# Kernel tuning notes

Hardware: AMD Instinct MI355X
Metric: run time of the kernel (lower is better)

Reference implementation:

```python
import jax, jax.numpy as jnp
import numpy as np
from jax import lax

# Shared Conv2d [1,1] + BN + ReLU is represented as a per-point affine (BN folded
# into conv weight/bias at eval) followed by ReLU, matching inference-mode math.

B, N1, N2, K = 8, 8192, 2048, 8
C1, C2 = 64, 128
MLP0, MLP1, MLP2 = 128, 128, 128  # mlp=[128,128], mlp2=[128]


def setup_inputs() -> dict:
    key = jax.random.key(0)
    ks = jax.random.split(key, 10)
    sc = lambda fan_in: 1.0 / np.sqrt(fan_in)
    return {
        "xyz1": jax.random.normal(ks[0], (B, N1, 3), jnp.float32),
        "xyz2": jax.random.normal(ks[1], (B, N2, 3), jnp.float32),
        "feat1": jax.random.normal(ks[2], (B, N1, C1), jnp.float32),
        "feat2": jax.random.normal(ks[3], (B, N2, C2), jnp.float32),
        "W0": jax.random.normal(ks[4], (C2 + 3, MLP0), jnp.float32) * sc(C2 + 3),
        "b0": jnp.zeros((MLP0,), jnp.float32),
        "W1": jax.random.normal(ks[5], (MLP0, MLP1), jnp.float32) * sc(MLP0),
        "b1": jnp.zeros((MLP1,), jnp.float32),
        "W2": jax.random.normal(ks[6], (MLP1 + C1, MLP2), jnp.float32) * sc(MLP1 + C1),
        "b2": jnp.zeros((MLP2,), jnp.float32),
    }


def _knn_idx(xyz1, xyz2, k):
    # squared distances (B, N1, N2); top-k nearest in xyz2 for each xyz1 point
    d2 = jnp.sum((xyz1[:, :, None, :] - xyz2[:, None, :, :]) ** 2, axis=-1)
    _, idx = lax.top_k(-d2, k)  # (B, N1, K)
    return idx


def _gather(src, idx):
    # src: (B, N2, C), idx: (B, N1, K) -> (B, N1, K, C)
    return jax.vmap(lambda s, i: s[i])(src, idx)


def reference(xyz1, xyz2, feat1, feat2, W0, b0, W1, b1, W2, b2):
    idx = _knn_idx(xyz1, xyz2, K)
    xyz2_g = _gather(xyz2, idx)            # (B, N1, K, 3)
    feat2_g = _gather(feat2, idx)          # (B, N1, K, C2)
    xyz_diff = xyz2_g - xyz1[:, :, None, :]
    net = jnp.concatenate([feat2_g, xyz_diff], axis=-1)  # (B, N1, K, C2+3)
    net = jax.nn.relu(net @ W0 + b0)
    net = jax.nn.relu(net @ W1 + b1)       # (B, N1, K, MLP1)
    pooled = jnp.max(net, axis=2)          # max pooling over neighbors
    cat = jnp.concatenate([pooled, feat1], axis=-1)      # (B, N1, MLP1+C1)
    out = jax.nn.relu(cat @ W2 + b2)       # (B, N1, MLP2)
    return out
```

## Files before the change

kernel.cpp:

```cpp
#include <hip/hip_runtime.h>
#include <hip/hip_bf16.h>

constexpr int B_  = 8;
constexpr int N1_ = 8192;
constexpr int N2_ = 2048;
constexpr int K_  = 8;

typedef short bf16x8 __attribute__((ext_vector_type(8)));
typedef float f32x4  __attribute__((ext_vector_type(4)));
typedef float f32x2  __attribute__((ext_vector_type(2)));

__device__ __forceinline__ short f2b(float x) {
    __hip_bfloat16 h = __float2bfloat16(x);
    return *reinterpret_cast<short*>(&h);
}

#define CASF(a, b) { const float _lo = fminf(a, b); \
                     const float _hi = fmaxf(a, b); \
                     (a) = _lo; (b) = _hi; }

__global__ __launch_bounds__(256) void prep_all(
    const float* __restrict__ feat2, short* __restrict__ feat2b,
    const float* __restrict__ W0, const float* __restrict__ W1,
    const float* __restrict__ W2, const float* __restrict__ xyz2,
    short* __restrict__ W0T, short* __restrict__ W1T, short* __restrict__ W2T,
    float* __restrict__ xp) {
    if (blockIdx.x < 2048) {
        const int i = blockIdx.x * 256 + threadIdx.x;
        const float4 v = ((const float4*)feat2)[i];
        uint2 o;
        o.x = (unsigned short)f2b(v.x) | ((unsigned)(unsigned short)f2b(v.y) << 16);
        o.y = (unsigned short)f2b(v.z) | ((unsigned)(unsigned short)f2b(v.w) << 16);
        ((uint2*)feat2b)[i] = o;
        return;
    }
    int i = (blockIdx.x - 2048) * 256 + threadIdx.x;
    if (i < 128 * 160) {
        const int n = i / 160, k = i % 160;
        W0T[i] = (k < 131) ? f2b(W0[k * 128 + n]) : (short)0;
        return;
    }
    i -= 128 * 160;
    if (i < 128 * 128) {
        const int n = i >> 7, k = i & 127;
        W1T[i] = f2b(W1[k * 128 + n]);
        return;
    }
    i -= 128 * 128;
    if (i < 128 * 192) {
        const int n = i / 192, k = i % 192;
        W2T[i] = f2b(W2[k * 128 + n]);
        return;
    }
    i -= 128 * 192;
    const int b = i >> 11, j = i & 2047;
    const float* src = xyz2 + ((size_t)b * N2_ + j) * 3;
    float* dst = xp + (size_t)b * 3 * N2_ + j;
    dst[0]        = src[0];
    dst[N2_]      = src[1];
    dst[2 * N2_]  = src[2];
}

constexpr int LCAP = 76;

__global__ __launch_bounds__(256) void knn_lazy(const float* __restrict__ xyz1,
                                                const float* __restrict__ xp,
                                                int* __restrict__ idx) {
    __shared__ __align__(16) unsigned short sMem[78 * 256];
    float* sD = (float*)sMem;
    int*   sI = (int*)sMem + 64 * 33;

    const int b = blockIdx.y;
    const int lane = threadIdx.x & 63;
    const int s = threadIdx.x >> 6;
    const int tid = threadIdx.x;
    const int n = blockIdx.x * 64 + lane;

    const float* q = xyz1 + ((size_t)b * N1_ + n) * 3;
    const float qx = q[0], qy = q[1], qz = q[2];
    const float* xs = xp + (size_t)b * 3 * N2_ + s * 512;
    const float* ys = xs + N2_;
    const float* zs = xs + 2 * N2_;

    float bd[K_];
#pragma unroll
    for (int t = 0; t < K_; ++t) bd[t] = 3.0e38f;
    int cnt = 0;

    const f32x2 qx2 = {qx, qx}, qy2 = {qy, qy}, qz2 = {qz, qz};

    for (int j0 = 0; j0 < 512; j0 += 8) {
        const float4 X0 = *(const float4*)(xs + j0);
        const float4 X1 = *(const float4*)(xs + j0 + 4);
        const float4 Y0 = *(const float4*)(ys + j0);
        const float4 Y1 = *(const float4*)(ys + j0 + 4);
        const float4 Z0 = *(const float4*)(zs + j0);
        const float4 Z1 = *(const float4*)(zs + j0 + 4);
        float xf[8];
        {
            f32x2 dx, dy, dz, d;
            dx = qx2 - f32x2{X0.x, X0.y}; dy = qy2 - f32x2{Y0.x, Y0.y}; dz = qz2 - f32x2{Z0.x, Z0.y};
            d = dx * dx + dy * dy + dz * dz; xf[0] = d.x; xf[1] = d.y;
            dx = qx2 - f32x2{X0.z, X0.w}; dy = qy2 - f32x2{Y0.z, Y0.w}; dz = qz2 - f32x2{Z0.z, Z0.w};
            d = dx * dx + dy * dy + dz * dz; xf[2] = d.x; xf[3] = d.y;
            dx = qx2 - f32x2{X1.x, X1.y}; dy = qy2 - f32x2{Y1.x, Y1.y}; dz = qz2 - f32x2{Z1.x, Z1.y};
            d = dx * dx + dy * dy + dz * dz; xf[4] = d.x; xf[5] = d.y;
            dx = qx2 - f32x2{X1.z, X1.w}; dy = qy2 - f32x2{Y1.z, Y1.w}; dz = qz2 - f32x2{Z1.z, Z1.w};
            d = dx * dx + dy * dy + dz * dz; xf[6] = d.x; xf[7] = d.y;
        }
        const float thr = bd[K_ - 1] * 1.0000038f;
#pragma unroll
        for (int u = 0; u < 8; ++u) {
            const bool acc = xf[u] < thr;
            if (acc) {
                const int capped = cnt < LCAP ? cnt : LCAP;
                sMem[capped * 256 + tid] = (unsigned short)(j0 + u);
                cnt++;
            }
        }
        CASF(xf[0], xf[1]); CASF(xf[2], xf[3]); CASF(xf[4], xf[5]); CASF(xf[6], xf[7]);
        CASF(xf[0], xf[2]); CASF(xf[1], xf[3]); CASF(xf[4], xf[6]); CASF(xf[5], xf[7]);
        CASF(xf[1], xf[2]); CASF(xf[5], xf[6]); CASF(xf[0], xf[4]); CASF(xf[3], xf[7]);
        CASF(xf[1], xf[5]); CASF(xf[2], xf[6]);
        CASF(xf[1], xf[4]); CASF(xf[3], xf[6]);
        CASF(xf[2], xf[4]); CASF(xf[3], xf[5]);
        CASF(xf[3], xf[4]);
        float t0 = fminf(bd[0], xf[7]);
        float t1 = fminf(bd[1], xf[6]);
        float t2 = fminf(bd[2], xf[5]);
        float t3 = fminf(bd[3], xf[4]);
        float t4 = fminf(bd[4], xf[3]);
        float t5 = fminf(bd[5], xf[2]);
        float t6 = fminf(bd[6], xf[1]);
        float t7 = fminf(bd[7], xf[0]);
        CASF(t0, t4); CASF(t1, t5); CASF(t2, t6); CASF(t3, t7);
        CASF(t0, t2); CASF(t1, t3); CASF(t4, t6); CASF(t5, t7);
        CASF(t0, t1); CASF(t2, t3); CASF(t4, t5); CASF(t6, t7);
        bd[0] = t0; bd[1] = t1; bd[2] = t2; bd[3] = t3;
        bd[4] = t4; bd[5] = t5; bd[6] = t6; bd[7] = t7;
    }

    float rd[K_];
    int   ri[K_];
#pragma unroll
    for (int t = 0; t < K_; ++t) { rd[t] = 3.0e38f; ri[t] = 0; }
    const int m = cnt < LCAP ? cnt : LCAP;
    for (int t = 0;; ++t) {
        const bool act = t < m;
        if (!__any(act)) break;
        if (act) {
#pragma clang fp contract(off)
            const int jl = sMem[t * 256 + tid];
            const float dx = qx - xs[jl];
            const float dy = qy - ys[jl];
            const float dz = qz - zs[jl];
            const float dx2 = dx * dx;
            const float dy2 = dy * dy;
            const float dz2 = dz * dz;
            const float d2 = (dx2 + dy2) + dz2;
            if (d2 < rd[K_ - 1]) {
                rd[K_ - 1] = d2; ri[K_ - 1] = s * 512 + jl;
#pragma unroll
                for (int t2 = K_ - 1; t2 >= 1; --t2) {
                    if (rd[t2] < rd[t2 - 1]) {
                        float td = rd[t2]; rd[t2] = rd[t2 - 1]; rd[t2 - 1] = td;
                        int   ti = ri[t2]; ri[t2] = ri[t2 - 1]; ri[t2 - 1] = ti;
                    }
                }
            }
        }
    }

    if (__any(cnt > LCAP)) {
        if (cnt > LCAP) {
#pragma unroll
            for (int t = 0; t < K_; ++t) { rd[t] = 3.0e38f; ri[t] = 0; }
            for (int j = 0; j < 512; ++j) {
#pragma clang fp contract(off)
                const float dx = qx - xs[j];
                const float dy = qy - ys[j];
                const float dz = qz - zs[j];
                const float dx2 = dx * dx;
                const float dy2 = dy * dy;
                const float dz2 = dz * dz;
                const float d2 = (dx2 + dy2) + dz2;
                if (d2 < rd[K_ - 1]) {
                    rd[K_ - 1] = d2; ri[K_ - 1] = s * 512 + j;
#pragma unroll
                    for (int t2 = K_ - 1; t2 >= 1; --t2) {
                        if (rd[t2] < rd[t2 - 1]) {
                            float td = rd[t2]; rd[t2] = rd[t2 - 1]; rd[t2 - 1] = td;
                            int   ti = ri[t2]; ri[t2] = ri[t2 - 1]; ri[t2 - 1] = ti;
                        }
                    }
                }
            }
        }
    }

    __syncthreads();
#pragma unroll
    for (int t = 0; t < K_; ++t) {
        sD[lane * 33 + s * 8 + t] = rd[t];
        sI[lane * 33 + s * 8 + t] = ri[t];
    }
    __syncthreads();

    if (tid < 64) {
        const int qq = tid;
        int h[4] = {0, 0, 0, 0};
        const int base = (b * N1_ + n) * K_;
#pragma unroll
        for (int t = 0; t < K_; ++t) {
            float best = 3.1e38f;
            int   bidx = 0, bs = 0;
#pragma unroll
            for (int ss = 0; ss < 4; ++ss) {
                if (h[ss] < 8) {
                    const float d = sD[qq * 33 + ss * 8 + h[ss]];
                    if (d < best) { best = d; bidx = sI[qq * 33 + ss * 8 + h[ss]]; bs = ss; }
                }
            }
#pragma unroll
            for (int ss = 0; ss < 4; ++ss) h[ss] += (ss == bs) ? 1 : 0;
            idx[base + t] = bidx;
        }
    }
}

__global__ __launch_bounds__(256) void fused_mfma(
    const float* __restrict__ xyz1, const float* __restrict__ xyz2,
    const float* __restrict__ feat1,
    const float* __restrict__ b0, const float* __restrict__ b1,
    const float* __restrict__ b2,
    const short* __restrict__ feat2b, const short* __restrict__ W0T,
    const short* __restrict__ W1T, const short* __restrict__ W2T,
    const int* __restrict__ idx, float* __restrict__ out) {
    __shared__ __align__(16) short sA[128 * 168];
    __shared__ __align__(16) short sCat[16 * 200];

    const int b = blockIdx.y;
    const int n0 = blockIdx.x * 16;
    const int tid = threadIdx.x;

    {
        const int row = tid >> 1, half = tid & 1;
        const int p = row >> 3, kk = row & 7;
        const int n = n0 + p;
        const int j = idx[((size_t)b * N1_ + n) * K_ + kk];
        const uint4* src = (const uint4*)(feat2b + ((size_t)(b * N2_ + j)) * 128 + half * 64);
        uint4* dst = (uint4*)(sA + row * 168 + half * 64);
#pragma unroll
        for (int t = 0; t < 8; ++t) dst[t] = src[t];
        uint4* pad = (uint4*)(sA + row * 168 + 128 + half * 16);
        if (half == 0) {
            const float dx = xyz2[((size_t)b * N2_ + j) * 3 + 0] - xyz1[((size_t)b * N1_ + n) * 3 + 0];
            const float dy = xyz2[((size_t)b * N2_ + j) * 3 + 1] - xyz1[((size_t)b * N1_ + n) * 3 + 1];
            const float dz = xyz2[((size_t)b * N2_ + j) * 3 + 2] - xyz1[((size_t)b * N1_ + n) * 3 + 2];
            uint4 v;
            v.x = (unsigned short)f2b(dx) | ((unsigned)(unsigned short)f2b(dy) << 16);
            v.y = (unsigned short)f2b(dz);
            v.z = 0; v.w = 0;
            pad[0] = v;
            pad[1] = make_uint4(0, 0, 0, 0);
        } else {
            pad[0] = make_uint4(0, 0, 0, 0);
            pad[1] = make_uint4(0, 0, 0, 0);
        }
    }
    {
#pragma unroll
        for (int u = 0; u < 4; ++u) {
            const int e = tid * 4 + u;
            const int p = e >> 6, c = e & 63;
            sCat[p * 200 + 128 + c] = f2b(feat1[((size_t)b * N1_ + n0 + p) * 64 + c]);
        }
    }
    __syncthreads();

    const int wave = tid >> 6, lane = tid & 63;
    const int q = lane >> 4, l15 = lane & 15;
    const int mBase = (wave & 1) * 64, nBase = (wave >> 1) * 64;

    const f32x4 zero4 = {0.f, 0.f, 0.f, 0.f};

    f32x4 acc[4][4];
#pragma unroll
    for (int mt = 0; mt < 4; ++mt)
#pragma unroll
        for (int nt = 0; nt < 4; ++nt) acc[mt][nt] = zero4;

    for (int ks = 0; ks < 5; ++ks) {
        bf16x8 af[4], bf[4];
#pragma unroll
        for (int mt = 0; mt < 4; ++mt)
            af[mt] = *(const bf16x8*)(sA + (mBase + mt * 16 + l15) * 168 + ks * 32 + q * 8);
#pragma unroll
        for (int nt = 0; nt < 4; ++nt)
            bf[nt] = *(const bf16x8*)(W0T + (nBase + nt * 16 + l15) * 160 + ks * 32 + q * 8);
#pragma unroll
        for (int mt = 0; mt < 4; ++mt)
#pragma unroll
            for (int nt = 0; nt < 4; ++nt)
                acc[mt][nt] = __builtin_amdgcn_mfma_f32_16x16x32_bf16(af[mt], bf[nt], acc[mt][nt], 0, 0, 0);
    }

    float b0v[4];
#pragma unroll
    for (int nt = 0; nt < 4; ++nt) b0v[nt] = b0[nBase + nt * 16 + l15];
    __syncthreads();
#pragma unroll
    for (int mt = 0; mt < 4; ++mt)
#pragma unroll
        for (int nt = 0; nt < 4; ++nt)
#pragma unroll
            for (int r = 0; r < 4; ++r) {
                const int row = mBase + mt * 16 + q * 4 + r;
                const int col = nBase + nt * 16 + l15;
                sA[row * 136 + col] = f2b(fmaxf(acc[mt][nt][r] + b0v[nt], 0.0f));
            }
    __syncthreads();

    f32x4 acc2[4][4];
#pragma unroll
    for (int mt = 0; mt < 4; ++mt)
#pragma unroll
        for (int nt = 0; nt < 4; ++nt) acc2[mt][nt] = zero4;

    for (int ks = 0; ks < 4; ++ks) {
        bf16x8 af[4], bf[4];
#pragma unroll
        for (int mt = 0; mt < 4; ++mt)
            af[mt] = *(const bf16x8*)(sA + (mBase + mt * 16 + l15) * 136 + ks * 32 + q * 8);
#pragma unroll
        for (int nt = 0; nt < 4; ++nt)
            bf[nt] = *(const bf16x8*)(W1T + (nBase + nt * 16 + l15) * 128 + ks * 32 + q * 8);
#pragma unroll
        for (int mt = 0; mt < 4; ++mt)
#pragma unroll
            for (int nt = 0; nt < 4; ++nt)
                acc2[mt][nt] = __builtin_amdgcn_mfma_f32_16x16x32_bf16(af[mt], bf[nt], acc2[mt][nt], 0, 0, 0);
    }

    float b1v[4];
#pragma unroll
    for (int nt = 0; nt < 4; ++nt) b1v[nt] = b1[nBase + nt * 16 + l15];
#pragma unroll
    for (int mt = 0; mt < 4; ++mt)
#pragma unroll
        for (int nt = 0; nt < 4; ++nt) {
            float vm = fmaxf(acc2[mt][nt][0] + b1v[nt], 0.0f);
#pragma unroll
            for (int r = 1; r < 4; ++r) vm = fmaxf(vm, acc2[mt][nt][r] + b1v[nt]);
            const float other = __shfl_xor(vm, 16);
            const float pool = fmaxf(vm, other);
            if ((q & 1) == 0) {
                const int pp = (mBase >> 3) + mt * 2 + (q >> 1);
                sCat[pp * 200 + nBase + nt * 16 + l15] = f2b(pool);
            }
        }
    __syncthreads();

    f32x4 acc3[2];
    acc3[0] = zero4; acc3[1] = zero4;
    const int nB2 = wave * 32;
    for (int ks = 0; ks < 6; ++ks) {
        const bf16x8 a2 = *(const bf16x8*)(sCat + l15 * 200 + ks * 32 + q * 8);
#pragma unroll
        for (int nt = 0; nt < 2; ++nt) {
            const bf16x8 b2f = *(const bf16x8*)(W2T + (nB2 + nt * 16 + l15) * 192 + ks * 32 + q * 8);
            acc3[nt] = __builtin_amdgcn_mfma_f32_16x16x32_bf16(a2, b2f, acc3[nt], 0, 0, 0);
        }
    }
    float b2v[2];
#pragma unroll
    for (int nt = 0; nt < 2; ++nt) b2v[nt] = b2[nB2 + nt * 16 + l15];
#pragma unroll
    for (int nt = 0; nt < 2; ++nt)
#pragma unroll
        for (int r = 0; r < 4; ++r) {
            const int p = q * 4 + r;
            const int col = nB2 + nt * 16 + l15;
            out[((size_t)(b * N1_ + n0 + p)) * 128 + col] = fmaxf(acc3[nt][r] + b2v[nt], 0.0f);
        }
}

extern "C" void kernel_launch(void* const* d_in, const int* in_sizes, int n_in,
                              void* d_out, int out_size, void* d_ws, size_t ws_size,
                              hipStream_t stream) {
    const float* xyz1  = (const float*)d_in[0];
    const float* xyz2  = (const float*)d_in[1];
    const float* feat1 = (const float*)d_in[2];
    const float* feat2 = (const float*)d_in[3];
    const float* W0    = (const float*)d_in[4];
    const float* b0    = (const float*)d_in[5];
    const float* W1    = (const float*)d_in[6];
    const float* b1    = (const float*)d_in[7];
    const float* W2    = (const float*)d_in[8];
    const float* b2    = (const float*)d_in[9];
    float* out = (float*)d_out;

    char* ws = (char*)d_ws;
    int*    idx    = (int*)(ws + 0);
    short*  feat2b = (short*)(ws + 2097152);
    short*  W0T    = (short*)(ws + 6291456);
    short*  W1T    = (short*)(ws + 6332416);
    short*  W2T    = (short*)(ws + 6365184);
    float*  xp     = (float*)(ws + 6414336);

    prep_all<<<2352, 256, 0, stream>>>(feat2, feat2b, W0, W1, W2, xyz2,
                                       W0T, W1T, W2T, xp);
    knn_lazy<<<dim3(N1_ / 64, B_), 256, 0, stream>>>(xyz1, xp, idx);
    fused_mfma<<<dim3(N1_ / 16, B_), 256, 0, stream>>>(xyz1, xyz2, feat1, b0, b1, b2,
                                                       feat2b, W0T, W1T, W2T, idx, out);
}
```

Measured before the change: 315.5 us.

## Fuse kNN search and MLP into one kernel keeping indices in shared memory

Merges the kNN kernel and the MFMA MLP kernel into a single kernel. Each block finds neighbours for 64 query points, keeps the indices in shared memory, then runs the MLP over four 16-point sub-tiles while reusing the same shared buffer. This removes the global idx round trip and one kernel launch. In exchange, the MLP phase runs at only 1024 blocks with serialized sub-tiles, and the kNN and MLP phases can no longer overlap across blocks with different resource needs. A launch-bounds occupancy hint of 3 blocks is added.

```diff
diff --git a/kernel.cpp b/kernel.cpp
--- a/kernel.cpp
+++ b/kernel.cpp
@@ -63,129 +63,112 @@
 
 constexpr int LCAP = 76;
 
-__global__ __launch_bounds__(256) void knn_lazy(const float* __restrict__ xyz1,
-                                                const float* __restrict__ xp,
-                                                int* __restrict__ idx) {
-    __shared__ __align__(16) unsigned short sMem[78 * 256];
-    float* sD = (float*)sMem;
-    int*   sI = (int*)sMem + 64 * 33;
+__global__ __launch_bounds__(256, 3) void knn_mlp(
+    const float* __restrict__ xyz1, const float* __restrict__ xp,
+    const float* __restrict__ xyz2, const float* __restrict__ feat1,
+    const float* __restrict__ b0, const float* __restrict__ b1,
+    const float* __restrict__ b2,
+    const short* __restrict__ feat2b, const short* __restrict__ W0T,
+    const short* __restrict__ W1T, const short* __restrict__ W2T,
+    float* __restrict__ out) {
+    __shared__ __align__(16) unsigned char sU[49408];
+    __shared__ __align__(16) unsigned short sIdx[512];
 
     const int b = blockIdx.y;
-    const int lane = threadIdx.x & 63;
-    const int s = threadIdx.x >> 6;
     const int tid = threadIdx.x;
-    const int n = blockIdx.x * 64 + lane;
-
-    const float* q = xyz1 + ((size_t)b * N1_ + n) * 3;
-    const float qx = q[0], qy = q[1], qz = q[2];
-    const float* xs = xp + (size_t)b * 3 * N2_ + s * 512;
-    const float* ys = xs + N2_;
-    const float* zs = xs + 2 * N2_;
-
-    float bd[K_];
-#pragma unroll
-    for (int t = 0; t < K_; ++t) bd[t] = 3.0e38f;
-    int cnt = 0;
-
-    const f32x2 qx2 = {qx, qx}, qy2 = {qy, qy}, qz2 = {qz, qz};
-
-    for (int j0 = 0; j0 < 512; j0 += 8) {
-        const float4 X0 = *(const float4*)(xs + j0);
-        const float4 X1 = *(const float4*)(xs + j0 + 4);
-        const float4 Y0 = *(const float4*)(ys + j0);
-        const float4 Y1 = *(const float4*)(ys + j0 + 4);
-        const float4 Z0 = *(const float4*)(zs + j0);
-        const float4 Z1 = *(const float4*)(zs + j0 + 4);
-        float xf[8];
-        {
-            f32x2 dx, dy, dz, d;
-            dx = qx2 - f32x2{X0.x, X0.y}; dy = qy2 - f32x2{Y0.x, Y0.y}; dz = qz2 - f32x2{Z0.x, Z0.y};
-            d = dx * dx + dy * dy + dz * dz; xf[0] = d.x; xf[1] = d.y;
-            dx = qx2 - f32x2{X0.z, X0.w}; dy = qy2 - f32x2{Y0.z, Y0.w}; dz = qz2 - f32x2{Z0.z, Z0.w};
-            d = dx * dx + dy * dy + dz * dz; xf[2] = d.x; xf[3] = d.y;
-            dx = qx2 - f32x2{X1.x, X1.y}; dy = qy2 - f32x2{Y1.x, Y1.y}; dz = qz2 - f32x2{Z1.x, Z1.y};
-            d = dx * dx + dy * dy + dz * dz; xf[4] = d.x; xf[5] = d.y;
-            dx = qx2 - f32x2{X1.z, X1.w}; dy = qy2 - f32x2{Y1.z, Y1.w}; dz = qz2 - f32x2{Z1.z, Z1.w};
-            d = dx * dx + dy * dy + dz * dz; xf[6] = d.x; xf[7] = d.y;
-        }
-        const float thr = bd[K_ - 1] * 1.0000038f;
-#pragma unroll
-        for (int u = 0; u < 8; ++u) {
-            const bool acc = xf[u] < thr;
-            if (acc) {
-                const int capped = cnt < LCAP ? cnt : LCAP;
-                sMem[capped * 256 + tid] = (unsigned short)(j0 + u);
-                cnt++;
-            }
-        }
-        CASF(xf[0], xf[1]); CASF(xf[2], xf[3]); CASF(xf[4], xf[5]); CASF(xf[6], xf[7]);
-        CASF(xf[0], xf[2]); CASF(xf[1], xf[3]); CASF(xf[4], xf[6]); CASF(xf[5], xf[7]);
-        CASF(xf[1], xf[2]); CASF(xf[5], xf[6]); CASF(xf[0], xf[4]); CASF(xf[3], xf[7]);
-        CASF(xf[1], xf[5]); CASF(xf[2], xf[6]);
-        CASF(xf[1], xf[4]); CASF(xf[3], xf[6]);
-        CASF(xf[2], xf[4]); CASF(xf[3], xf[5]);
-        CASF(xf[3], xf[4]);
-        float t0 = fminf(bd[0], xf[7]);
-        float t1 = fminf(bd[1], xf[6]);
-        float t2 = fminf(bd[2], xf[5]);
-        float t3 = fminf(bd[3], xf[4]);
-        float t4 = fminf(bd[4], xf[3]);
-        float t5 = fminf(bd[5], xf[2]);
-        float t6 = fminf(bd[6], xf[1]);
-        float t7 = fminf(bd[7], xf[0]);
-        CASF(t0, t4); CASF(t1, t5); CASF(t2, t6); CASF(t3, t7);
-        CASF(t0, t2); CASF(t1, t3); CASF(t4, t6); CASF(t5, t7);
-        CASF(t0, t1); CASF(t2, t3); CASF(t4, t5); CASF(t6, t7);
-        bd[0] = t0; bd[1] = t1; bd[2] = t2; bd[3] = t3;
-        bd[4] = t4; bd[5] = t5; bd[6] = t6; bd[7] = t7;
-    }
-
-    float rd[K_];
-    int   ri[K_];
-#pragma unroll
-    for (int t = 0; t < K_; ++t) { rd[t] = 3.0e38f; ri[t] = 0; }
-    const int m = cnt < LCAP ? cnt : LCAP;
-    for (int t = 0;; ++t) {
-        const bool act = t < m;
-        if (!__any(act)) break;
-        if (act) {
+    const int lane = tid & 63;
+
+    {
+        unsigned short* sMem = (unsigned short*)sU;
+        float* sD = (float*)sU;
+        int*   sI = (int*)sU + 64 * 33;
+        const int s = tid >> 6;
+        const int n = blockIdx.x * 64 + lane;
+
+        const float* qp = xyz1 + ((size_t)b * N1_ + n) * 3;
+        const float qx = qp[0], qy = qp[1], qz = qp[2];
+        const float* xs = xp + (size_t)b * 3 * N2_ + s * 512;
+        const float* ys = xs + N2_;
+        const float* zs = xs + 2 * N2_;
+
+        float bd[K_];
+#pragma unroll
+        for (int t = 0; t < K_; ++t) bd[t] = 3.0e38f;
+        int cnt = 0;
+
+        const f32x2 qx2 = {qx, qx}, qy2 = {qy, qy}, qz2 = {qz, qz};
+
+        for (int j0 = 0; j0 < 512; j0 += 8) {
+            const float4 X0 = *(const float4*)(xs + j0);
+            const float4 X1 = *(const float4*)(xs + j0 + 4);
+            const float4 Y0 = *(const float4*)(ys + j0);
+            const float4 Y1 = *(const float4*)(ys + j0 + 4);
+            const float4 Z0 = *(const float4*)(zs + j0);
+            const float4 Z1 = *(const float4*)(zs + j0 + 4);
+            float xf[8];
+            {
+                f32x2 dx, dy, dz, d;
+                dx = qx2 - f32x2{X0.x, X0.y}; dy = qy2 - f32x2{Y0.x, Y0.y}; dz = qz2 - f32x2{Z0.x, Z0.y};
+                d = dx * dx + dy * dy + dz * dz; xf[0] = d.x; xf[1] = d.y;
+                dx = qx2 - f32x2{X0.z, X0.w}; dy = qy2 - f32x2{Y0.z, Y0.w}; dz = qz2 - f32x2{Z0.z, Z0.w};
+                d = dx * dx + dy * dy + dz * dz; xf[2] = d.x; xf[3] = d.y;
+                dx = qx2 - f32x2{X1.x, X1.y}; dy = qy2 - f32x2{Y1.x, Y1.y}; dz = qz2 - f32x2{Z1.x, Z1.y};
+                d = dx * dx + dy * dy + dz * dz; xf[4] = d.x; xf[5] = d.y;
+                dx = qx2 - f32x2{X1.z, X1.w}; dy = qy2 - f32x2{Y1.z, Y1.w}; dz = qz2 - f32x2{Z1.z, Z1.w};
+                d = dx * dx + dy * dy + dz * dz; xf[6] = d.x; xf[7] = d.y;
+            }
+            const float thr = bd[K_ - 1] * 1.0000038f;
+#pragma unroll
+            for (int u = 0; u < 8; ++u) {
+                const bool acc = xf[u] < thr;
+                if (acc) {
+                    const int capped = cnt < LCAP ? cnt : LCAP;
+                    sMem[capped * 256 + tid] = (unsigned short)(j0 + u);
+                    cnt++;
+                }
+            }
+            CASF(xf[0], xf[1]); CASF(xf[2], xf[3]); CASF(xf[4], xf[5]); CASF(xf[6], xf[7]);
+            CASF(xf[0], xf[2]); CASF(xf[1], xf[3]); CASF(xf[4], xf[6]); CASF(xf[5], xf[7]);
+            CASF(xf[1], xf[2]); CASF(xf[5], xf[6]); CASF(xf[0], xf[4]); CASF(xf[3], xf[7]);
+            CASF(xf[1], xf[5]); CASF(xf[2], xf[6]);
+            CASF(xf[1], xf[4]); CASF(xf[3], xf[6]);
+            CASF(xf[2], xf[4]); CASF(xf[3], xf[5]);
+            CASF(xf[3], xf[4]);
+            float t0 = fminf(bd[0], xf[7]);
+            float t1 = fminf(bd[1], xf[6]);
+            float t2 = fminf(bd[2], xf[5]);
+            float t3 = fminf(bd[3], xf[4]);
+            float t4 = fminf(bd[4], xf[3]);
+            float t5 = fminf(bd[5], xf[2]);
+            float t6 = fminf(bd[6], xf[1]);
+            float t7 = fminf(bd[7], xf[0]);
+            CASF(t0, t4); CASF(t1, t5); CASF(t2, t6); CASF(t3, t7);
+            CASF(t0, t2); CASF(t1, t3); CASF(t4, t6); CASF(t5, t7);
+            CASF(t0, t1); CASF(t2, t3); CASF(t4, t5); CASF(t6, t7);
+            bd[0] = t0; bd[1] = t1; bd[2] = t2; bd[3] = t3;
+            bd[4] = t4; bd[5] = t5; bd[6] = t6; bd[7] = t7;
+        }
+
+        float rd[K_];
+        int   ri[K_];
+#pragma unroll
+        for (int t = 0; t < K_; ++t) { rd[t] = 3.0e38f; ri[t] = 0; }
+        const int m = cnt < LCAP ? cnt : LCAP;
+        for (int t = 0;; ++t) {
+            const bool act = t < m;
+            if (!__any(act)) break;
+            if (act) {
 #pragma clang fp contract(off)
-            const int jl = sMem[t * 256 + tid];
-            const float dx = qx - xs[jl];
-            const float dy = qy - ys[jl];
-            const float dz = qz - zs[jl];
-            const float dx2 = dx * dx;
-            const float dy2 = dy * dy;
-            const float dz2 = dz * dz;
-            const float d2 = (dx2 + dy2) + dz2;
-            if (d2 < rd[K_ - 1]) {
-                rd[K_ - 1] = d2; ri[K_ - 1] = s * 512 + jl;
-#pragma unroll
-                for (int t2 = K_ - 1; t2 >= 1; --t2) {
-                    if (rd[t2] < rd[t2 - 1]) {
-                        float td = rd[t2]; rd[t2] = rd[t2 - 1]; rd[t2 - 1] = td;
-                        int   ti = ri[t2]; ri[t2] = ri[t2 - 1]; ri[t2 - 1] = ti;
-                    }
-                }
-            }
-        }
-    }
-
-    if (__any(cnt > LCAP)) {
-        if (cnt > LCAP) {
-#pragma unroll
-            for (int t = 0; t < K_; ++t) { rd[t] = 3.0e38f; ri[t] = 0; }
-            for (int j = 0; j < 512; ++j) {
-#pragma clang fp contract(off)
-                const float dx = qx - xs[j];
-                const float dy = qy - ys[j];
-                const float dz = qz - zs[j];
+                const int jl = sMem[t * 256 + tid];
+                const float dx = qx - xs[jl];
+                const float dy = qy - ys[jl];
+                const float dz = qz - zs[jl];
                 const float dx2 = dx * dx;
                 const float dy2 = dy * dy;
                 const float dz2 = dz * dz;
                 const float d2 = (dx2 + dy2) + dz2;
                 if (d2 < rd[K_ - 1]) {
-                    rd[K_ - 1] = d2; ri[K_ - 1] = s * 512 + j;
+                    rd[K_ - 1] = d2; ri[K_ - 1] = s * 512 + jl;
 #pragma unroll
                     for (int t2 = K_ - 1; t2 >= 1; --t2) {
                         if (rd[t2] < rd[t2 - 1]) {
@@ -196,193 +179,209 @@
                 }
             }
         }
-    }
-
-    __syncthreads();
-#pragma unroll
-    for (int t = 0; t < K_; ++t) {
-        sD[lane * 33 + s * 8 + t] = rd[t];
-        sI[lane * 33 + s * 8 + t] = ri[t];
-    }
-    __syncthreads();
-
-    if (tid < 64) {
-        const int qq = tid;
-        int h[4] = {0, 0, 0, 0};
-        const int base = (b * N1_ + n) * K_;
+
+        if (__any(cnt > LCAP)) {
+            if (cnt > LCAP) {
+#pragma unroll
+                for (int t = 0; t < K_; ++t) { rd[t] = 3.0e38f; ri[t] = 0; }
+                for (int j = 0; j < 512; ++j) {
+#pragma clang fp contract(off)
+                    const float dx = qx - xs[j];
+                    const float dy = qy - ys[j];
+                    const float dz = qz - zs[j];
+                    const float dx2 = dx * dx;
+                    const float dy2 = dy * dy;
+                    const float dz2 = dz * dz;
+                    const float d2 = (dx2 + dy2) + dz2;
+                    if (d2 < rd[K_ - 1]) {
+                        rd[K_ - 1] = d2; ri[K_ - 1] = s * 512 + j;
+#pragma unroll
+                        for (int t2 = K_ - 1; t2 >= 1; --t2) {
+                            if (rd[t2] < rd[t2 - 1]) {
+                                float td = rd[t2]; rd[t2] = rd[t2 - 1]; rd[t2 - 1] = td;
+                                int   ti = ri[t2]; ri[t2] = ri[t2 - 1]; ri[t2 - 1] = ti;
+                            }
+                        }
+                    }
+                }
+            }
+        }
+
+        __syncthreads();
 #pragma unroll
         for (int t = 0; t < K_; ++t) {
-            float best = 3.1e38f;
-            int   bidx = 0, bs = 0;
-#pragma unroll
-            for (int ss = 0; ss < 4; ++ss) {
-                if (h[ss] < 8) {
-                    const float d = sD[qq * 33 + ss * 8 + h[ss]];
-                    if (d < best) { best = d; bidx = sI[qq * 33 + ss * 8 + h[ss]]; bs = ss; }
-                }
-            }
-#pragma unroll
-            for (int ss = 0; ss < 4; ++ss) h[ss] += (ss == bs) ? 1 : 0;
-            idx[base + t] = bidx;
-        }
-    }
-}
-
-__global__ __launch_bounds__(256) void fused_mfma(
-    const float* __restrict__ xyz1, const float* __restrict__ xyz2,
-    const float* __restrict__ feat1,
-    const float* __restrict__ b0, const float* __restrict__ b1,
-    const float* __restrict__ b2,
-    const short* __restrict__ feat2b, const short* __restrict__ W0T,
-    const short* __restrict__ W1T, const short* __restrict__ W2T,
-    const int* __restrict__ idx, float* __restrict__ out) {
-    __shared__ __align__(16) short sA[128 * 168];
-    __shared__ __align__(16) short sCat[16 * 200];
-
-    const int b = blockIdx.y;
-    const int n0 = blockIdx.x * 16;
-    const int tid = threadIdx.x;
-
-    {
-        const int row = tid >> 1, half = tid & 1;
-        const int p = row >> 3, kk = row & 7;
-        const int n = n0 + p;
-        const int j = idx[((size_t)b * N1_ + n) * K_ + kk];
-        const uint4* src = (const uint4*)(feat2b + ((size_t)(b * N2_ + j)) * 128 + half * 64);
-        uint4* dst = (uint4*)(sA + row * 168 + half * 64);
-#pragma unroll
-        for (int t = 0; t < 8; ++t) dst[t] = src[t];
-        uint4* pad = (uint4*)(sA + row * 168 + 128 + half * 16);
-        if (half == 0) {
-            const float dx = xyz2[((size_t)b * N2_ + j) * 3 + 0] - xyz1[((size_t)b * N1_ + n) * 3 + 0];
-            const float dy = xyz2[((size_t)b * N2_ + j) * 3 + 1] - xyz1[((size_t)b * N1_ + n) * 3 + 1];
-            const float dz = xyz2[((size_t)b * N2_ + j) * 3 + 2] - xyz1[((size_t)b * N1_ + n) * 3 + 2];
-            uint4 v;
-            v.x = (unsigned short)f2b(dx) | ((unsigned)(unsigned short)f2b(dy) << 16);
-            v.y = (unsigned short)f2b(dz);
-            v.z = 0; v.w = 0;
-            pad[0] = v;
-            pad[1] = make_uint4(0, 0, 0, 0);
-        } else {
-            pad[0] = make_uint4(0, 0, 0, 0);
-            pad[1] = make_uint4(0, 0, 0, 0);
-        }
-    }
-    {
-#pragma unroll
-        for (int u = 0; u < 4; ++u) {
-            const int e = tid * 4 + u;
-            const int p = e >> 6, c = e & 63;
-            sCat[p * 200 + 128 + c] = f2b(feat1[((size_t)b * N1_ + n0 + p) * 64 + c]);
-        }
-    }
-    __syncthreads();
-
-    const int wave = tid >> 6, lane = tid & 63;
-    const int q = lane >> 4, l15 = lane & 15;
+            sD[lane * 33 + s * 8 + t] = rd[t];
+            sI[lane * 33 + s * 8 + t] = ri[t];
+        }
+        __syncthreads();
+
+        if (tid < 64) {
+            const int qq = tid;
+            int h[4] = {0, 0, 0, 0};
+#pragma unroll
+            for (int t = 0; t < K_; ++t) {
+                float best = 3.1e38f;
+                int   bidx = 0, bs = 0;
+#pragma unroll
+                for (int ss = 0; ss < 4; ++ss) {
+                    if (h[ss] < 8) {
+                        const float d = sD[qq * 33 + ss * 8 + h[ss]];
+                        if (d < best) { best = d; bidx = sI[qq * 33 + ss * 8 + h[ss]]; bs = ss; }
+                    }
+                }
+#pragma unroll
+                for (int ss = 0; ss < 4; ++ss) h[ss] += (ss == bs) ? 1 : 0;
+                sIdx[qq * 8 + t] = (unsigned short)bidx;
+            }
+        }
+    }
+
+    short* sA   = (short*)sU;
+    short* sCat = (short*)(sU + 43008);
+    const int wave = tid >> 6;
+    const int qd = lane >> 4, l15 = lane & 15;
     const int mBase = (wave & 1) * 64, nBase = (wave >> 1) * 64;
-
     const f32x4 zero4 = {0.f, 0.f, 0.f, 0.f};
 
-    f32x4 acc[4][4];
-#pragma unroll
-    for (int mt = 0; mt < 4; ++mt)
-#pragma unroll
-        for (int nt = 0; nt < 4; ++nt) acc[mt][nt] = zero4;
-
-    for (int ks = 0; ks < 5; ++ks) {
-        bf16x8 af[4], bf[4];
+    for (int it = 0; it < 4; ++it) {
+        const int n0 = blockIdx.x * 64 + it * 16;
+        __syncthreads();
+
+        {
+            const int row = tid >> 1, half = tid & 1;
+            const int p = row >> 3, kk = row & 7;
+            const int n = n0 + p;
+            const int j = sIdx[(it * 16 + p) * 8 + kk];
+            const uint4* src = (const uint4*)(feat2b + ((size_t)(b * N2_ + j)) * 128 + half * 64);
+            uint4* dst = (uint4*)(sA + row * 168 + half * 64);
+#pragma unroll
+            for (int t = 0; t < 8; ++t) dst[t] = src[t];
+            uint4* pad = (uint4*)(sA + row * 168 + 128 + half * 16);
+            if (half == 0) {
+                const float dx = xyz2[((size_t)b * N2_ + j) * 3 + 0] - xyz1[((size_t)b * N1_ + n) * 3 + 0];
+                const float dy = xyz2[((size_t)b * N2_ + j) * 3 + 1] - xyz1[((size_t)b * N1_ + n) * 3 + 1];
+                const float dz = xyz2[((size_t)b * N2_ + j) * 3 + 2] - xyz1[((size_t)b * N1_ + n) * 3 + 2];
+                uint4 v;
+                v.x = (unsigned short)f2b(dx) | ((unsigned)(unsigned short)f2b(dy) << 16);
+                v.y = (unsigned short)f2b(dz);
+                v.z = 0; v.w = 0;
+                pad[0] = v;
+                pad[1] = make_uint4(0, 0, 0, 0);
+            } else {
+                pad[0] = make_uint4(0, 0, 0, 0);
+                pad[1] = make_uint4(0, 0, 0, 0);
+            }
+        }
+        {
+#pragma unroll
+            for (int u = 0; u < 4; ++u) {
+                const int e = tid * 4 + u;
+                const int p = e >> 6, c = e & 63;
+                sCat[p * 200 + 128 + c] = f2b(feat1[((size_t)b * N1_ + n0 + p) * 64 + c]);
+            }
+        }
+        __syncthreads();
+
+        f32x4 acc[4][4];
 #pragma unroll
         for (int mt = 0; mt < 4; ++mt)
-            af[mt] = *(const bf16x8*)(sA + (mBase + mt * 16 + l15) * 168 + ks * 32 + q * 8);
-#pragma unroll
-        for (int nt = 0; nt < 4; ++nt)
-            bf[nt] = *(const bf16x8*)(W0T + (nBase + nt * 16 + l15) * 160 + ks * 32 + q * 8);
+#pragma unroll
+            for (int nt = 0; nt < 4; ++nt) acc[mt][nt] = zero4;
+
+        for (int ks = 0; ks < 5; ++ks) {
+            bf16x8 af[4], bf[4];
+#pragma unroll
+            for (int mt = 0; mt < 4; ++mt)
+                af[mt] = *(const bf16x8*)(sA + (mBase + mt * 16 + l15) * 168 + ks * 32 + qd * 8);
+#pragma unroll
+            for (int nt = 0; nt < 4; ++nt)
+                bf[nt] = *(const bf16x8*)(W0T + (nBase + nt * 16 + l15) * 160 + ks * 32 + qd * 8);
+#pragma unroll
+            for (int mt = 0; mt < 4; ++mt)
+#pragma unroll
+                for (int nt = 0; nt < 4; ++nt)
+                    acc[mt][nt] = __builtin_amdgcn_mfma_f32_16x16x32_bf16(af[mt], bf[nt], acc[mt][nt], 0, 0, 0);
+        }
+
+        float b0v[4];
+#pragma unroll
+        for (int nt = 0; nt < 4; ++nt) b0v[nt] = b0[nBase + nt * 16 + l15];
+        __syncthreads();
 #pragma unroll
         for (int mt = 0; mt < 4; ++mt)
 #pragma unroll
             for (int nt = 0; nt < 4; ++nt)
-                acc[mt][nt] = __builtin_amdgcn_mfma_f32_16x16x32_bf16(af[mt], bf[nt], acc[mt][nt], 0, 0, 0);
-    }
-
-    float b0v[4];
-#pragma unroll
-    for (int nt = 0; nt < 4; ++nt) b0v[nt] = b0[nBase + nt * 16 + l15];
-    __syncthreads();
-#pragma unroll
-    for (int mt = 0; mt < 4; ++mt)
-#pragma unroll
-        for (int nt = 0; nt < 4; ++nt)
+#pragma unroll
+                for (int r = 0; r < 4; ++r) {
+                    const int row = mBase + mt * 16 + qd * 4 + r;
+                    const int col = nBase + nt * 16 + l15;
+                    sA[row * 136 + col] = f2b(fmaxf(acc[mt][nt][r] + b0v[nt], 0.0f));
+                }
+        __syncthreads();
+
+        f32x4 acc2[4][4];
+#pragma unroll
+        for (int mt = 0; mt < 4; ++mt)
+#pragma unroll
+            for (int nt = 0; nt < 4; ++nt) acc2[mt][nt] = zero4;
+
+        for (int ks = 0; ks < 4; ++ks) {
+            bf16x8 af[4], bf[4];
+#pragma unroll
+            for (int mt = 0; mt < 4; ++mt)
+                af[mt] = *(const bf16x8*)(sA + (mBase + mt * 16 + l15) * 136 + ks * 32 + qd * 8);
+#pragma unroll
+            for (int nt = 0; nt < 4; ++nt)
+                bf[nt] = *(const bf16x8*)(W1T + (nBase + nt * 16 + l15) * 128 + ks * 32 + qd * 8);
+#pragma unroll
+            for (int mt = 0; mt < 4; ++mt)
+#pragma unroll
+                for (int nt = 0; nt < 4; ++nt)
+                    acc2[mt][nt] = __builtin_amdgcn_mfma_f32_16x16x32_bf16(af[mt], bf[nt], acc2[mt][nt], 0, 0, 0);
+        }
+
+        float b1v[4];
+#pragma unroll
+        for (int nt = 0; nt < 4; ++nt) b1v[nt] = b1[nBase + nt * 16 + l15];
+#pragma unroll
+        for (int mt = 0; mt < 4; ++mt)
+#pragma unroll
+            for (int nt = 0; nt < 4; ++nt) {
+                float vm = fmaxf(acc2[mt][nt][0] + b1v[nt], 0.0f);
+#pragma unroll
+                for (int r = 1; r < 4; ++r) vm = fmaxf(vm, acc2[mt][nt][r] + b1v[nt]);
+                const float other = __shfl_xor(vm, 16);
+                const float pool = fmaxf(vm, other);
+                if ((qd & 1) == 0) {
+                    const int pp = (mBase >> 3) + mt * 2 + (qd >> 1);
+                    sCat[pp * 200 + nBase + nt * 16 + l15] = f2b(pool);
+                }
+            }
+        __syncthreads();
+
+        f32x4 acc3[2];
+        acc3[0] = zero4; acc3[1] = zero4;
+        const int nB2 = wave * 32;
+        for (int ks = 0; ks < 6; ++ks) {
+            const bf16x8 a2 = *(const bf16x8*)(sCat + l15 * 200 + ks * 32 + qd * 8);
+#pragma unroll
+            for (int nt = 0; nt < 2; ++nt) {
+                const bf16x8 b2f = *(const bf16x8*)(W2T + (nB2 + nt * 16 + l15) * 192 + ks * 32 + qd * 8);
+                acc3[nt] = __builtin_amdgcn_mfma_f32_16x16x32_bf16(a2, b2f, acc3[nt], 0, 0, 0);
+            }
+        }
+        float b2v[2];
+#pragma unroll
+        for (int nt = 0; nt < 2; ++nt) b2v[nt] = b2[nB2 + nt * 16 + l15];
+#pragma unroll
+        for (int nt = 0; nt < 2; ++nt)
 #pragma unroll
             for (int r = 0; r < 4; ++r) {
-                const int row = mBase + mt * 16 + q * 4 + r;
-                const int col = nBase + nt * 16 + l15;
-                sA[row * 136 + col] = f2b(fmaxf(acc[mt][nt][r] + b0v[nt], 0.0f));
-            }
-    __syncthreads();
-
-    f32x4 acc2[4][4];
-#pragma unroll
-    for (int mt = 0; mt < 4; ++mt)
-#pragma unroll
-        for (int nt = 0; nt < 4; ++nt) acc2[mt][nt] = zero4;
-
-    for (int ks = 0; ks < 4; ++ks) {
-        bf16x8 af[4], bf[4];
-#pragma unroll
-        for (int mt = 0; mt < 4; ++mt)
-            af[mt] = *(const bf16x8*)(sA + (mBase + mt * 16 + l15) * 136 + ks * 32 + q * 8);
-#pragma unroll
-        for (int nt = 0; nt < 4; ++nt)
-            bf[nt] = *(const bf16x8*)(W1T + (nBase + nt * 16 + l15) * 128 + ks * 32 + q * 8);
-#pragma unroll
-        for (int mt = 0; mt < 4; ++mt)
-#pragma unroll
-            for (int nt = 0; nt < 4; ++nt)
-                acc2[mt][nt] = __builtin_amdgcn_mfma_f32_16x16x32_bf16(af[mt], bf[nt], acc2[mt][nt], 0, 0, 0);
-    }
-
-    float b1v[4];
-#pragma unroll
-    for (int nt = 0; nt < 4; ++nt) b1v[nt] = b1[nBase + nt * 16 + l15];
-#pragma unroll
-    for (int mt = 0; mt < 4; ++mt)
-#pragma unroll
-        for (int nt = 0; nt < 4; ++nt) {
-            float vm = fmaxf(acc2[mt][nt][0] + b1v[nt], 0.0f);
-#pragma unroll
-            for (int r = 1; r < 4; ++r) vm = fmaxf(vm, acc2[mt][nt][r] + b1v[nt]);
-            const float other = __shfl_xor(vm, 16);
-            const float pool = fmaxf(vm, other);
-            if ((q & 1) == 0) {
-                const int pp = (mBase >> 3) + mt * 2 + (q >> 1);
-                sCat[pp * 200 + nBase + nt * 16 + l15] = f2b(pool);
-            }
-        }
-    __syncthreads();
-
-    f32x4 acc3[2];
-    acc3[0] = zero4; acc3[1] = zero4;
-    const int nB2 = wave * 32;
-    for (int ks = 0; ks < 6; ++ks) {
-        const bf16x8 a2 = *(const bf16x8*)(sCat + l15 * 200 + ks * 32 + q * 8);
-#pragma unroll
-        for (int nt = 0; nt < 2; ++nt) {
-            const bf16x8 b2f = *(const bf16x8*)(W2T + (nB2 + nt * 16 + l15) * 192 + ks * 32 + q * 8);
-            acc3[nt] = __builtin_amdgcn_mfma_f32_16x16x32_bf16(a2, b2f, acc3[nt], 0, 0, 0);
-        }
-    }
-    float b2v[2];
-#pragma unroll
-    for (int nt = 0; nt < 2; ++nt) b2v[nt] = b2[nB2 + nt * 16 + l15];
-#pragma unroll
-    for (int nt = 0; nt < 2; ++nt)
-#pragma unroll
-        for (int r = 0; r < 4; ++r) {
-            const int p = q * 4 + r;
-            const int col = nB2 + nt * 16 + l15;
-            out[((size_t)(b * N1_ + n0 + p)) * 128 + col] = fmaxf(acc3[nt][r] + b2v[nt], 0.0f);
-        }
+                const int p = qd * 4 + r;
+                const int col = nB2 + nt * 16 + l15;
+                out[((size_t)(b * N1_ + n0 + p)) * 128 + col] = fmaxf(acc3[nt][r] + b2v[nt], 0.0f);
+            }
+    }
 }
 
 extern "C" void kernel_launch(void* const* d_in, const int* in_sizes, int n_in,
@@ -401,16 +400,15 @@
     float* out = (float*)d_out;
 
     char* ws = (char*)d_ws;
-    int*    idx    = (int*)(ws + 0);
-    short*  feat2b = (short*)(ws + 2097152);
-    short*  W0T    = (short*)(ws + 6291456);
-    short*  W1T    = (short*)(ws + 6332416);
-    short*  W2T    = (short*)(ws + 6365184);
-    float*  xp     = (float*)(ws + 6414336);
+    short*  feat2b = (short*)(ws);
+    short*  W0T    = (short*)(ws + 4194304);
+    short*  W1T    = (short*)(ws + 4235264);
+    short*  W2T    = (short*)(ws + 4268032);
+    float*  xp     = (float*)(ws + 4317184);
 
     prep_all<<<2352, 256, 0, stream>>>(feat2, feat2b, W0, W1, W2, xyz2,
                                        W0T, W1T, W2T, xp);
-    knn_lazy<<<dim3(N1_ / 64, B_), 256, 0, stream>>>(xyz1, xp, idx);
-    fused_mfma<<<dim3(N1_ / 16, B_), 256, 0, stream>>>(xyz1, xyz2, feat1, b0, b1, b2,
-                                                       feat2b, W0T, W1T, W2T, idx, out);
+    knn_mlp<<<dim3(N1_ / 64, B_), 256, 0, stream>>>(xyz1, xp, xyz2, feat1,
+                                                    b0, b1, b2, feat2b,
+                                                    W0T, W1T, W2T, out);
 }
```

Result: slower. 405.6 us (+28.6%).
